# Optimization experiments

Measured on AMD Instinct MI355X. Metric: run time of the kernel, lower is better.

The kernel has to match this reference:

```python
import jax, jax.numpy as jnp
import numpy as np

N_NODES = 100000
N_EDGES = 1600000
NODE_F = 25
HID = 128
LN_EPS = 1e-5


def _mlp_ln(h, w1, b1, w2, b2, w3, b3, g, beta):
    # Linear -> ReLU -> Linear -> ReLU -> Linear -> LayerNorm
    h = jax.nn.relu(h @ w1 + b1)
    h = jax.nn.relu(h @ w2 + b2)
    h = h @ w3 + b3
    mu = jnp.mean(h, axis=-1, keepdims=True)
    var = jnp.mean(jnp.square(h - mu), axis=-1, keepdims=True)
    return (h - mu) * jax.lax.rsqrt(var + LN_EPS) * g + beta


def setup_inputs() -> dict:
    key = jax.random.key(0)
    ks = jax.random.split(key, 10)
    x = jax.random.normal(ks[0], (N_NODES, NODE_F), dtype=jnp.float32)
    edge_index = jax.random.randint(ks[1], (2, N_EDGES), 0, N_NODES, dtype=jnp.int64)

    def lin(k, fin, fout):
        s = 1.0 / np.sqrt(fin)
        kw, kb = jax.random.split(k)
        w = jax.random.uniform(kw, (fin, fout), jnp.float32, -s, s)
        b = jax.random.uniform(kb, (fout,), jnp.float32, -s, s)
        return w, b

    ew1, eb1 = lin(ks[2], 4, HID)
    ew2, eb2 = lin(ks[3], HID, HID)
    ew3, eb3 = lin(ks[4], HID, HID)
    nw1, nb1 = lin(ks[5], NODE_F, HID)
    nw2, nb2 = lin(ks[6], HID, HID)
    nw3, nb3 = lin(ks[7], HID, HID)
    eg = jnp.ones((HID,), jnp.float32); ebeta = jnp.zeros((HID,), jnp.float32)
    ng = jnp.ones((HID,), jnp.float32); nbeta = jnp.zeros((HID,), jnp.float32)
    return dict(x=x, edge_index=edge_index,
                ew1=ew1, eb1=eb1, ew2=ew2, eb2=eb2, ew3=ew3, eb3=eb3, eg=eg, ebeta=ebeta,
                nw1=nw1, nb1=nb1, nw2=nw2, nb2=nb2, nw3=nw3, nb3=nb3, ng=ng, nbeta=nbeta)


def reference(x, edge_index, ew1, eb1, ew2, eb2, ew3, eb3, eg, ebeta,
              nw1, nb1, nw2, nb2, nw3, nb3, ng, nbeta):
    row, col = edge_index[0], edge_index[1]
    # edge model: gather src/dest positions, relative displacement + magnitude
    distance = x[row, 0:3] - x[col, 0:3]                      # [E, 3]
    magnitude = jnp.linalg.norm(distance, axis=1, keepdims=True)  # [E, 1]
    edge_in = jnp.concatenate([distance, magnitude], axis=1)  # [E, 4]
    edge_out = _mlp_ln(edge_in, ew1, eb1, ew2, eb2, ew3, eb3, eg, ebeta)  # [E, 128]
    # node model: MLP over raw x (the masked copy in the original is unused)
    node_out = _mlp_ln(x, nw1, nb1, nw2, nb2, nw3, nb3, ng, nbeta)  # [N, 128]
    return node_out, edge_out
```

## Files before the change

### kernel.cpp

```cpp
#include <hip/hip_runtime.h>

#define E_EDGES 1600000
#define N_NODES_ 100000

typedef unsigned short u16;
typedef unsigned int u32;
typedef short bf16x8 __attribute__((ext_vector_type(8)));
typedef u16 u16x4 __attribute__((ext_vector_type(4)));
typedef float f32x4 __attribute__((ext_vector_type(4)));

__device__ __forceinline__ u16 f2bf(float f){
  u32 u = __builtin_bit_cast(u32, f);
  u += 0x7fffu + ((u >> 16) & 1u);
  return (u16)(u >> 16);
}

__global__ void pack4(const float* __restrict__ a, const float* __restrict__ b,
                      const float* __restrict__ c, const float* __restrict__ d,
                      u16* __restrict__ pa, u16* __restrict__ pb,
                      u16* __restrict__ pc, u16* __restrict__ pd){
  int tid = blockIdx.x * 256 + threadIdx.x;
  int mat = tid >> 11, rem = tid & 2047;
  int n = rem >> 8, k = (rem >> 6) & 3, lane = rem & 63;
  const float* w = mat==0 ? a : mat==1 ? b : mat==2 ? c : d;
  u16* p       = mat==0 ? pa : mat==1 ? pb : mat==2 ? pc : pd;
  int rbase = k*32 + (lane>>4)*8;
  int col   = n*16 + (lane&15);
  int o = ((n*4 + k)*64 + lane)*8;
  #pragma unroll
  for (int j=0;j<8;++j) p[o+j] = f2bf(w[(rbase+j)*128 + col]);
}

__global__ void pack_xyz(const float* __restrict__ x, float4* __restrict__ xyz, int n){
  int i = blockIdx.x * 256 + threadIdx.x;
  if (i < n){
    const float* p = x + (long)i*25;
    float4 v; v.x = p[0]; v.y = p[1]; v.z = p[2]; v.w = 0.f;
    xyz[i] = v;
  }
}

template<int IS_EDGE>
__global__ __launch_bounds__(256, 4)
void encoder_kernel(const float* __restrict__ x, const int* __restrict__ eidx,
                    const float4* __restrict__ xyz,
                    const float* __restrict__ w1, const float* __restrict__ b1,
                    const u16* __restrict__ pw2, const float* __restrict__ b2,
                    const u16* __restrict__ pw3, const float* __restrict__ b3,
                    const float* __restrict__ gw, const float* __restrict__ bw,
                    float* __restrict__ out, long outbase, int nrows, int ntiles)
{
  constexpr int K1  = IS_EDGE ? 4 : 25;
  constexpr int K1P = IS_EDGE ? 4 : 26;
  constexpr int W1F = K1 * 128;

  __shared__ __align__(16) float w1s[W1F];
  __shared__ __align__(16) float b1s[128];
  __shared__ __align__(16) float in_s[64*K1P];
  __shared__ __align__(16) unsigned char h12s[16384];
  __shared__ __align__(16) float pts[64*8];

  const int tid  = threadIdx.x;
  const int lane = tid & 63, wave = tid >> 6;
  const int li = lane & 15, lg = lane >> 4;
  const int wbase = wave * 32;

  bf16x8 W2f[2][4], W3f[2][4];
  #pragma unroll
  for (int mt=0;mt<2;++mt)
    #pragma unroll
    for (int kc=0;kc<4;++kc){
      W2f[mt][kc] = *(const bf16x8*)(pw2 + (((wave*2+mt)*4 + kc)*64 + lane)*8);
      W3f[mt][kc] = *(const bf16x8*)(pw3 + (((wave*2+mt)*4 + kc)*64 + lane)*8);
    }
  f32x4 b2q[2];
  #pragma unroll
  for (int mt=0;mt<2;++mt)
    b2q[mt] = *(const f32x4*)(b2 + wbase + mt*16 + lg*4);
  asm volatile("" ::: "memory");

  for (int i = tid; i < W1F/4; i += 256)
    ((float4*)w1s)[i] = ((const float4*)w1)[i];
  if (tid < 32) ((float4*)b1s)[tid] = ((const float4*)b1)[tid];

  float4 curg = {0.f,0.f,0.f,0.f};
  int ni0 = 0, ni1 = 0;
  float4 nr4 = {0.f,0.f,0.f,0.f}, nc4 = {0.f,0.f,0.f,0.f};
  if (IS_EDGE && tid < 64){
    int t0 = blockIdx.x;
    if (t0 < ntiles){
      long e = (long)t0*64 + tid;
      int ir = eidx[e], ic = eidx[E_EDGES + e];
      float4 a = xyz[ir], b = xyz[ic];
      float dx = a.x-b.x, dy = a.y-b.y, dz = a.z-b.z;
      curg.x=dx; curg.y=dy; curg.z=dz; curg.w=sqrtf(dx*dx+dy*dy+dz*dz);
      int t1 = t0 + gridDim.x;
      if (t1 < ntiles){
        long e1 = (long)t1*64 + tid;
        ni0 = eidx[e1]; ni1 = eidx[E_EDGES + e1];
      }
    }
  }

  const f32x4 zv = {0.f,0.f,0.f,0.f};

  for (int tile = blockIdx.x; tile < ntiles; tile += gridDim.x){
    const int row0 = tile * 64;
    const bool hasnext = (tile + (int)gridDim.x) < ntiles;

    if (IS_EDGE){
      if (tid < 64){
        ((float4*)in_s)[tid] = curg;
        if (hasnext){
          nr4 = xyz[ni0]; nc4 = xyz[ni1];
          int t2 = tile + 2*(int)gridDim.x;
          if (t2 < ntiles){
            long e2 = (long)t2*64 + tid;
            ni0 = eidx[e2]; ni1 = eidx[E_EDGES + e2];
          }
        }
      }
    } else {
      for (int i = tid; i < 64*25; i += 256){
        int r = i / 25, k = i - r*25;
        float v = (row0 + r < nrows) ? x[(long)row0*25 + i] : 0.f;
        in_s[r*K1P + k] = v;
      }
    }
    __syncthreads();

    {
      const int r = tid >> 2, jb0 = (tid & 3) << 5;
      #pragma unroll
      for (int p=0;p<2;++p){
        const int jb = jb0 + p*16;
        float a1[16];
        #pragma unroll
        for (int j=0;j<16;++j) a1[j] = b1s[jb + j];
        for (int k=0;k<K1;++k){
          float xv = in_s[r*K1P + k];
          const float4* wr = (const float4*)(w1s + k*128 + jb);
          #pragma unroll
          for (int j4=0;j4<4;++j4){
            float4 wv = wr[j4];
            a1[j4*4+0] = fmaf(xv, wv.x, a1[j4*4+0]);
            a1[j4*4+1] = fmaf(xv, wv.y, a1[j4*4+1]);
            a1[j4*4+2] = fmaf(xv, wv.z, a1[j4*4+2]);
            a1[j4*4+3] = fmaf(xv, wv.w, a1[j4*4+3]);
          }
        }
        #pragma unroll
        for (int q=0;q<2;++q){
          bf16x8 pk;
          #pragma unroll
          for (int t=0;t<8;++t){
            float v = a1[q*8+t]; v = v > 0.f ? v : 0.f;
            pk[t] = (short)f2bf(v);
          }
          *(bf16x8*)(h12s + r*256 + ((((jb>>3)+q) ^ (r&7))<<4)) = pk;
        }
      }
    }
    __syncthreads();

    f32x4 acc[2][4];
    #pragma unroll
    for (int mt=0;mt<2;++mt)
      #pragma unroll
      for (int nt=0;nt<4;++nt) acc[mt][nt] = zv;
    #pragma unroll
    for (int kc=0;kc<4;++kc){
      #pragma unroll
      for (int nt=0;nt<4;++nt){
        bf16x8 hf = *(const bf16x8*)(h12s + (nt*16+li)*256 + (((kc*4+lg)^(li&7))<<4));
        acc[0][nt] = __builtin_amdgcn_mfma_f32_16x16x32_bf16(W2f[0][kc], hf, acc[0][nt], 0,0,0);
        acc[1][nt] = __builtin_amdgcn_mfma_f32_16x16x32_bf16(W2f[1][kc], hf, acc[1][nt], 0,0,0);
      }
    }

    if (IS_EDGE && tid < 64 && hasnext){
      float dx = nr4.x-nc4.x, dy = nr4.y-nc4.y, dz = nr4.z-nc4.z;
      curg.x=dx; curg.y=dy; curg.z=dz; curg.w=sqrtf(dx*dx+dy*dy+dz*dz);
    }

    __syncthreads();

    #pragma unroll
    for (int mt=0;mt<2;++mt){
      const int f0 = wbase + mt*16 + lg*4;
      #pragma unroll
      for (int nt=0;nt<4;++nt){
        u16x4 pk;
        #pragma unroll
        for (int j=0;j<4;++j){
          float v = acc[mt][nt][j] + b2q[mt][j];
          v = v > 0.f ? v : 0.f;
          pk[j] = f2bf(v);
        }
        const int r = nt*16 + li;
        *(u16x4*)(h12s + r*256 + (((f0>>3) ^ (r&7))<<4) + ((f0&7)<<1)) = pk;
      }
    }
    __syncthreads();

    #pragma unroll
    for (int mt=0;mt<2;++mt)
      #pragma unroll
      for (int nt=0;nt<4;++nt) acc[mt][nt] = zv;
    #pragma unroll
    for (int kc=0;kc<4;++kc){
      #pragma unroll
      for (int nt=0;nt<4;++nt){
        bf16x8 hf = *(const bf16x8*)(h12s + (nt*16+li)*256 + (((kc*4+lg)^(li&7))<<4));
        acc[0][nt] = __builtin_amdgcn_mfma_f32_16x16x32_bf16(W3f[0][kc], hf, acc[0][nt], 0,0,0);
        acc[1][nt] = __builtin_amdgcn_mfma_f32_16x16x32_bf16(W3f[1][kc], hf, acc[1][nt], 0,0,0);
      }
    }

    f32x4 b3q[2], gq[2], bq[2];
    #pragma unroll
    for (int mt=0;mt<2;++mt){
      b3q[mt] = *(const f32x4*)(b3 + wbase + mt*16 + lg*4);
      gq[mt]  = *(const f32x4*)(gw + wbase + mt*16 + lg*4);
      bq[mt]  = *(const f32x4*)(bw + wbase + mt*16 + lg*4);
    }

    float sA[4]  = {0.f,0.f,0.f,0.f};
    float sqA[4] = {0.f,0.f,0.f,0.f};
    #pragma unroll
    for (int mt=0;mt<2;++mt)
      #pragma unroll
      for (int nt=0;nt<4;++nt)
        #pragma unroll
        for (int j=0;j<4;++j){
          float v = acc[mt][nt][j] + b3q[mt][j];
          acc[mt][nt][j] = v;
          sA[nt] += v; sqA[nt] += v*v;
        }
    #pragma unroll
    for (int nt=0;nt<4;++nt){
      sA[nt]  += __shfl_xor(sA[nt], 16);  sA[nt]  += __shfl_xor(sA[nt], 32);
      sqA[nt] += __shfl_xor(sqA[nt], 16); sqA[nt] += __shfl_xor(sqA[nt], 32);
    }
    if (lg == 0){
      #pragma unroll
      for (int nt=0;nt<4;++nt){
        pts[(nt*16+li)*8 + wave*2]     = sA[nt];
        pts[(nt*16+li)*8 + wave*2 + 1] = sqA[nt];
      }
    }
    __syncthreads();

    #pragma unroll
    for (int nt=0;nt<4;++nt){
      const int r = nt*16 + li;
      f32x4 p0 = *(const f32x4*)(pts + r*8);
      f32x4 p1 = *(const f32x4*)(pts + r*8 + 4);
      float S  = p0[0]+p0[2]+p1[0]+p1[2];
      float SQ = p0[1]+p0[3]+p1[1]+p1[3];
      float mu = S * 0.0078125f;
      float rs = rsqrtf(SQ*0.0078125f - mu*mu + 1e-5f);
      const int grow = row0 + r;
      if (IS_EDGE || grow < nrows){
        #pragma unroll
        for (int mt=0;mt<2;++mt){
          f32x4 o;
          #pragma unroll
          for (int j=0;j<4;++j)
            o[j] = (acc[mt][nt][j]-mu)*rs*gq[mt][j] + bq[mt][j];
          *(f32x4*)(out + outbase + (long)grow*128 + wbase + mt*16 + lg*4) = o;
        }
      }
    }
  }
}

extern "C" void kernel_launch(void* const* d_in, const int* in_sizes, int n_in,
                              void* d_out, int out_size, void* d_ws, size_t ws_size,
                              hipStream_t stream){
  const float* x   = (const float*)d_in[0];
  const int*  eidx = (const int*)d_in[1];
  const float* ew1 = (const float*)d_in[2];
  const float* eb1 = (const float*)d_in[3];
  const float* ew2 = (const float*)d_in[4];
  const float* eb2 = (const float*)d_in[5];
  const float* ew3 = (const float*)d_in[6];
  const float* eb3 = (const float*)d_in[7];
  const float* eg  = (const float*)d_in[8];
  const float* ebt = (const float*)d_in[9];
  const float* nw1 = (const float*)d_in[10];
  const float* nb1 = (const float*)d_in[11];
  const float* nw2 = (const float*)d_in[12];
  const float* nb2 = (const float*)d_in[13];
  const float* nw3 = (const float*)d_in[14];
  const float* nb3 = (const float*)d_in[15];
  const float* ng  = (const float*)d_in[16];
  const float* nbt = (const float*)d_in[17];
  float* out = (float*)d_out;

  u16* pew2 = (u16*)d_ws;
  u16* pew3 = pew2 + 16384;
  u16* pnw2 = pew3 + 16384;
  u16* pnw3 = pnw2 + 16384;
  float4* xyz = (float4*)((char*)d_ws + 131072);

  pack4<<<32, 256, 0, stream>>>(ew2, ew3, nw2, nw3, pew2, pew3, pnw2, pnw3);
  pack_xyz<<<(N_NODES_ + 255)/256, 256, 0, stream>>>(x, xyz, N_NODES_);
  encoder_kernel<1><<<2048, 256, 0, stream>>>(x, eidx, xyz, ew1, eb1, pew2, eb2, pew3, eb3,
      eg, ebt, out, (long)N_NODES_ * 128, E_EDGES, E_EDGES/64);
  encoder_kernel<0><<<1024, 256, 0, stream>>>(x, nullptr, nullptr, nw1, nb1, pnw2, nb2, pnw3, nb3,
      ng, nbt, out, 0, N_NODES_, (N_NODES_ + 63)/64);
}
```

Before: 555.4 us.

## Stage LayerNorm output through LDS for coalesced row stores; pad W1 smem layout

```diff
diff --git a/kernel.cpp b/kernel.cpp
--- a/kernel.cpp
+++ b/kernel.cpp
@@ -52,13 +52,15 @@
 {
   constexpr int K1  = IS_EDGE ? 4 : 25;
   constexpr int K1P = IS_EDGE ? 4 : 26;
-  constexpr int W1F = K1 * 128;
-
-  __shared__ __align__(16) float w1s[W1F];
-  __shared__ __align__(16) float b1s[128];
+  constexpr int WGS = K1*32 + 4;
+  constexpr int SP  = 132;
+
+  __shared__ __align__(16) float w1s[4*WGS];
+  __shared__ __align__(16) float b1s[4*36];
   __shared__ __align__(16) float in_s[64*K1P];
   __shared__ __align__(16) unsigned char h12s[16384];
   __shared__ __align__(16) float pts[64*8];
+  __shared__ __align__(16) float stage[16*SP];
 
   const int tid  = threadIdx.x;
   const int lane = tid & 63, wave = tid >> 6;
@@ -79,9 +81,12 @@
     b2q[mt] = *(const f32x4*)(b2 + wbase + mt*16 + lg*4);
   asm volatile("" ::: "memory");
 
-  for (int i = tid; i < W1F/4; i += 256)
-    ((float4*)w1s)[i] = ((const float4*)w1)[i];
-  if (tid < 32) ((float4*)b1s)[tid] = ((const float4*)b1)[tid];
+  for (int i = tid; i < K1*32; i += 256){
+    int k = i >> 5, col = (i & 31) * 4;
+    float4 v = ((const float4*)w1)[i];
+    *(float4*)(w1s + (col>>5)*WGS + k*32 + (col&31)) = v;
+  }
+  if (tid < 128) b1s[(tid>>5)*36 + (tid&31)] = b1[tid];
 
   float4 curg = {0.f,0.f,0.f,0.f};
   int ni0 = 0, ni1 = 0;
@@ -134,12 +139,13 @@
       #pragma unroll
       for (int p=0;p<2;++p){
         const int jb = jb0 + p*16;
+        const int g = jb >> 5, go = jb & 31;
         float a1[16];
         #pragma unroll
-        for (int j=0;j<16;++j) a1[j] = b1s[jb + j];
+        for (int j=0;j<16;++j) a1[j] = b1s[g*36 + go + j];
         for (int k=0;k<K1;++k){
           float xv = in_s[r*K1P + k];
-          const float4* wr = (const float4*)(w1s + k*128 + jb);
+          const float4* wr = (const float4*)(w1s + g*WGS + k*32 + go);
           #pragma unroll
           for (int j4=0;j4<4;++j4){
             float4 wv = wr[j4];
@@ -251,25 +257,41 @@
     }
     __syncthreads();
 
+    const int cr  = tid >> 4;
+    const int ccol = (tid & 15) * 8;
+    float4 oreg[4][2];
     #pragma unroll
     for (int nt=0;nt<4;++nt){
-      const int r = nt*16 + li;
-      f32x4 p0 = *(const f32x4*)(pts + r*8);
-      f32x4 p1 = *(const f32x4*)(pts + r*8 + 4);
-      float S  = p0[0]+p0[2]+p1[0]+p1[2];
-      float SQ = p0[1]+p0[3]+p1[1]+p1[3];
-      float mu = S * 0.0078125f;
-      float rs = rsqrtf(SQ*0.0078125f - mu*mu + 1e-5f);
-      const int grow = row0 + r;
-      if (IS_EDGE || grow < nrows){
+      {
+        const int r = nt*16 + li;
+        f32x4 p0 = *(const f32x4*)(pts + r*8);
+        f32x4 p1 = *(const f32x4*)(pts + r*8 + 4);
+        float S  = p0[0]+p0[2]+p1[0]+p1[2];
+        float SQ = p0[1]+p0[3]+p1[1]+p1[3];
+        float mu = S * 0.0078125f;
+        float rs = rsqrtf(SQ*0.0078125f - mu*mu + 1e-5f);
         #pragma unroll
         for (int mt=0;mt<2;++mt){
           f32x4 o;
           #pragma unroll
           for (int j=0;j<4;++j)
             o[j] = (acc[mt][nt][j]-mu)*rs*gq[mt][j] + bq[mt][j];
-          *(f32x4*)(out + outbase + (long)grow*128 + wbase + mt*16 + lg*4) = o;
-        }
+          *(f32x4*)(stage + li*SP + wbase + mt*16 + lg*4) = o;
+        }
+      }
+      __syncthreads();
+      oreg[nt][0] = *(const float4*)(stage + cr*SP + ccol);
+      oreg[nt][1] = *(const float4*)(stage + cr*SP + ccol + 4);
+      if (nt < 3) __syncthreads();
+    }
+
+    #pragma unroll
+    for (int nt=0;nt<4;++nt){
+      const int grow = row0 + nt*16 + cr;
+      if (IS_EDGE || grow < nrows){
+        float* op = out + outbase + (long)grow*128 + ccol;
+        ((float4*)op)[0] = oreg[nt][0];
+        ((float4*)op)[1] = oreg[nt][1];
       }
     }
   }
@@ -306,8 +328,8 @@
 
   pack4<<<32, 256, 0, stream>>>(ew2, ew3, nw2, nw3, pew2, pew3, pnw2, pnw3);
   pack_xyz<<<(N_NODES_ + 255)/256, 256, 0, stream>>>(x, xyz, N_NODES_);
-  encoder_kernel<1><<<2048, 256, 0, stream>>>(x, eidx, xyz, ew1, eb1, pew2, eb2, pew3, eb3,
+  encoder_kernel<1><<<2500, 256, 0, stream>>>(x, eidx, xyz, ew1, eb1, pew2, eb2, pew3, eb3,
       eg, ebt, out, (long)N_NODES_ * 128, E_EDGES, E_EDGES/64);
-  encoder_kernel<0><<<1024, 256, 0, stream>>>(x, nullptr, nullptr, nw1, nb1, pnw2, nb2, pnw3, nb3,
+  encoder_kernel<0><<<521, 256, 0, stream>>>(x, nullptr, nullptr, nw1, nb1, pnw2, nb2, pnw3, nb3,
       ng, nbt, out, 0, N_NODES_, (N_NODES_ + 63)/64);
 }
```

Measured after the change: 728.2 us. 1.31x slower.
